# Performance work log

Measured on AMD Instinct MI355X. Metric: run time of the kernel, lower is better.

## Reference

```python
import jax, jax.numpy as jnp
import numpy as np

WIN = (7, 7)
NUM_HEADS = 6
DIM = 192
NW = 64          # windows per image
BATCH = 64       # images
B_ = BATCH * NW  # 4096 window-batches
N = WIN[0] * WIN[1]  # 49


def _relative_position_index():
    ch, cw = np.arange(WIN[0]), np.arange(WIN[1])
    coords = np.stack(np.meshgrid(ch, cw, indexing='ij'))          # [2, Wh, Ww]
    cf = coords.reshape(2, -1)                                      # [2, N]
    rel = cf[:, :, None] - cf[:, None, :]                           # [2, N, N]
    rel = rel.transpose(1, 2, 0).astype(np.int64)                   # [N, N, 2]
    rel[:, :, 0] += WIN[0] - 1
    rel[:, :, 1] += WIN[1] - 1
    rel[:, :, 0] *= 2 * WIN[1] - 1
    return rel.sum(-1).astype(np.int32)                             # [N, N]


def setup_inputs() -> dict:
    key = jax.random.key(0)
    ks = jax.random.split(key, 8)
    x = jax.random.normal(ks[0], (B_, N, DIM), dtype=jnp.float32)
    # additive shift-window mask: 0 where allowed, -100 where disallowed
    u = jax.random.uniform(ks[1], (NW, N, N))
    attn_mask = jnp.where(u < 0.15, -100.0, 0.0).astype(jnp.float32)
    rpb_table = jax.random.normal(ks[2], ((2 * WIN[0] - 1) * (2 * WIN[1] - 1), NUM_HEADS), dtype=jnp.float32) * 0.02
    rel_index = jnp.asarray(_relative_position_index())
    std = 1.0 / np.sqrt(DIM)
    qkv_w = jax.random.normal(ks[3], (3 * DIM, DIM), dtype=jnp.float32) * std
    qkv_b = jax.random.normal(ks[4], (3 * DIM,), dtype=jnp.float32) * 0.02
    proj_w = jax.random.normal(ks[5], (DIM, DIM), dtype=jnp.float32) * std
    proj_b = jax.random.normal(ks[6], (DIM,), dtype=jnp.float32) * 0.02
    return {"x": x, "attn_mask": attn_mask, "rpb_table": rpb_table,
            "rel_index": rel_index, "qkv_w": qkv_w, "qkv_b": qkv_b,
            "proj_w": proj_w, "proj_b": proj_b}


def reference(x, attn_mask, rpb_table, rel_index, qkv_w, qkv_b, proj_w, proj_b):
    Bw, n, C = x.shape
    H = NUM_HEADS
    hd = C // H
    scale = hd ** -0.5
    # qkv projection: [Bw, N, 3, H, hd] -> (3, Bw, H, N, hd)
    qkv = (x @ qkv_w.T + qkv_b).reshape(Bw, n, 3, H, hd).transpose(2, 0, 3, 1, 4)
    q, k, v = qkv[0], qkv[1], qkv[2]
    # gathered relative position bias: [H, N, N]
    rel_bias = rpb_table[rel_index.reshape(-1)].reshape(n, n, H).transpose(2, 0, 1)
    # scores [Bw, H, N, N]
    attn = jnp.einsum('bhnd,bhmd->bhnm', q * scale, k) + rel_bias[None]
    nW = attn_mask.shape[0]
    attn = attn.reshape(Bw // nW, nW, H, n, n) + attn_mask[None, :, None]
    attn = jax.nn.softmax(attn.reshape(Bw, H, n, n), axis=-1)
    out = jnp.einsum('bhnm,bhmd->bhnd', attn, v)  # [Bw, H, N, hd]
    out = out.transpose(0, 2, 1, 3).reshape(Bw, n, C)
    return out @ proj_w.T + proj_b
```

## Files before the change

### kernel.cpp

```cpp
#include <hip/hip_runtime.h>
#include <stdint.h>
#include <cmath>

typedef unsigned short ushort_t;
typedef __attribute__((ext_vector_type(8))) short bf16x8;
typedef __attribute__((ext_vector_type(4))) float f32x4;
typedef __attribute__((ext_vector_type(4))) unsigned int u32x4;

#define NTOK 49
#define DIMC 192
#define NH 6
#define HD 32
#define SCALE 0.17677669529663687f
#define LOG2E 1.4426950408889634f
#define LN2   0.6931471805599453f
#define XS 200
#define VTS 72
#define PS 72
#define MS 66
#define RS 68

#define OFF_X    0
#define OFF_Q    25600
#define OFF_K    51200
#define OFF_VT   76800
#define OFF_P    104448
#define OFF_MASK 122880
#define OFF_RPB  139776
#define OFF_REL  145184
#define OFF_BQ   153888
#define OFF_BP   156192
#define SMEM_BYTES 156960

#define QKVW_N (576 * 192)
#define PROJW_N (192 * 192)
#define QKV_GRP (4 * 9 * 6 * 64)
#define PROJ_GRP (4 * 3 * 6 * 64)
#define WBF_BYTES ((QKVW_N + PROJW_N) * 2)
#define BIAS_FLOATS (64 * 6 * 4 * 4 * 4 * 16 * 4)
#define WS_NEED1 ((size_t)WBF_BYTES)
#define WS_NEED2 ((size_t)WBF_BYTES + (size_t)BIAS_FLOATS * 4)

__device__ __forceinline__ ushort_t f2bf(float f) {
    uint32_t x = __builtin_bit_cast(uint32_t, f);
    x += 0x7fffu + ((x >> 16) & 1u);
    return (ushort_t)(x >> 16);
}
__device__ __forceinline__ uint32_t cvtpk(float lo, float hi) {
    uint32_t r;
    asm("v_cvt_pk_bf16_f32 %0, %1, %2" : "=v"(r) : "v"(lo), "v"(hi));
    return r;
}

__device__ __forceinline__ bf16x8 cvt8(const float* p) {
    f32x4 a = *(const f32x4*)p;
    f32x4 b = *(const f32x4*)(p + 4);
    bf16x8 r;
    r[0] = (short)f2bf(a[0]); r[1] = (short)f2bf(a[1]);
    r[2] = (short)f2bf(a[2]); r[3] = (short)f2bf(a[3]);
    r[4] = (short)f2bf(b[0]); r[5] = (short)f2bf(b[1]);
    r[6] = (short)f2bf(b[2]); r[7] = (short)f2bf(b[3]);
    return r;
}

__global__ __launch_bounds__(256) void swz_weights_kernel(
    const float* __restrict__ qkvw, const float* __restrict__ projw,
    ushort_t* __restrict__ dst)
{
    int i = blockIdx.x * 256 + threadIdx.x;
    if (i >= QKV_GRP + PROJ_GRP) return;
    const float* src;
    float s = 1.0f;
    if (i < QKV_GRP) {
        int lane = i & 63, t = i >> 6;
        int kk = t % 6, nt = (t / 6) % 9, cq = t / 54;
        int col = cq * 144 + nt * 16 + (lane & 15);
        int k0 = kk * 32 + (lane >> 4) * 8;
        src = qkvw + col * DIMC + k0;
        if (col < 192) s = SCALE * LOG2E;
    } else {
        int j = i - QKV_GRP;
        int lane = j & 63, t = j >> 6;
        int kk = t % 6, nt = (t / 6) % 3, cq = t / 18;
        int col = cq * 48 + nt * 16 + (lane & 15);
        int k0 = kk * 32 + (lane >> 4) * 8;
        src = projw + col * DIMC + k0;
    }
    f32x4 a = *(const f32x4*)src;
    f32x4 b = *(const f32x4*)(src + 4);
    u32x4 o;
    o[0] = (uint32_t)f2bf(a[0] * s) | ((uint32_t)f2bf(a[1] * s) << 16);
    o[1] = (uint32_t)f2bf(a[2] * s) | ((uint32_t)f2bf(a[3] * s) << 16);
    o[2] = (uint32_t)f2bf(b[0] * s) | ((uint32_t)f2bf(b[1] * s) << 16);
    o[3] = (uint32_t)f2bf(b[2] * s) | ((uint32_t)f2bf(b[3] * s) << 16);
    *(u32x4*)(dst + (size_t)i * 8) = o;
}

__global__ __launch_bounds__(256) void bias_kernel(
    const float* __restrict__ mask_g, const float* __restrict__ rpb_g,
    const int* __restrict__ rel_g, float* __restrict__ dst)
{
    int i = blockIdx.x * 256 + threadIdx.x;
    if (i >= BIAS_FLOATS / 4) return;
    int c = i & 15, g = (i >> 4) & 3, t = (i >> 6) & 3, wsid = (i >> 8) & 3;
    int hw = i >> 10;
    int h = hw % 6, wi = hw / 6;
    int m0 = 16 * wsid + 4 * g, n = 16 * t + c;
    f32x4 v;
    #pragma unroll
    for (int r = 0; r < 4; ++r) {
        int m = m0 + r;
        float val;
        if (n >= NTOK)      val = -30000.0f;
        else if (m >= NTOK) val = 0.0f;
        else val = mask_g[(size_t)wi * (NTOK * NTOK) + m * NTOK + n]
                 + rpb_g[(size_t)rel_g[m * NTOK + n] * NH + h];
        v[r] = val * LOG2E;
    }
    *(f32x4*)(dst + (size_t)i * 4) = v;
}

template <int MODE>
__global__ __launch_bounds__(512, 2) void win_attn_kernel(
    const float* __restrict__ x_g,
    const float* __restrict__ mask_g,
    const float* __restrict__ rpb_g,
    const int* __restrict__ rel_g,
    const float* __restrict__ qkvw_g,
    const float* __restrict__ qkvb_g,
    const float* __restrict__ projw_g,
    const float* __restrict__ projb_g,
    const ushort_t* __restrict__ wbf_g,
    const float* __restrict__ bias_g,
    float* __restrict__ out_g)
{
    extern __shared__ char smem[];
    ushort_t* x_lds  = (ushort_t*)(smem + OFF_X);
    ushort_t* q_lds  = (ushort_t*)(smem + OFF_Q);
    ushort_t* k_lds  = (ushort_t*)(smem + OFF_K);
    ushort_t* vT     = (ushort_t*)(smem + OFF_VT);
    ushort_t* P_lds  = (ushort_t*)(smem + OFF_P);
    float*    mask_p = (float*)(smem + OFF_MASK);
    float*    rpb_l  = (float*)(smem + OFF_RPB);
    ushort_t* rel_p  = (ushort_t*)(smem + OFF_REL);
    float*    bq     = (float*)(smem + OFF_BQ);
    float*    bp     = (float*)(smem + OFF_BP);

    const int tid  = threadIdx.x;
    const int b    = blockIdx.x;
    const int wi   = b & 63;
    const int w    = tid >> 6;
    const int lane = tid & 63;
    const int g    = lane >> 4;
    const int c    = lane & 15;

    bf16x8 ring[4][6];
    {
        if constexpr (MODE >= 1) {
            const int cq = w & 3;
            const ushort_t* wq = wbf_g + (size_t)cq * (9 * 6 * 64 * 8);
            #pragma unroll
            for (int p = 0; p < 3; ++p)
                #pragma unroll
                for (int kk = 0; kk < 6; ++kk)
                    ring[p][kk] = *(const bf16x8*)(wq + (size_t)((p * 6 + kk) * 64 + lane) * 8);
            __builtin_amdgcn_sched_barrier(0);
        }
    }

    {
        const float* xg = x_g + (size_t)b * (NTOK * DIMC);
        for (int i = tid; i < 64 * 24; i += 512) {
            int row = i / 24, col = (i % 24) * 8;
            u32x4 v = {0u, 0u, 0u, 0u};
            if (row < NTOK) {
                const float* src = xg + row * DIMC + col;
                f32x4 a = *(const f32x4*)src;
                f32x4 d = *(const f32x4*)(src + 4);
                v[0] = cvtpk(a[0], a[1]); v[1] = cvtpk(a[2], a[3]);
                v[2] = cvtpk(d[0], d[1]); v[3] = cvtpk(d[2], d[3]);
            }
            *(u32x4*)&x_lds[row * XS + col] = v;
        }
        if constexpr (MODE < 2) {
            const float* mw = mask_g + (size_t)wi * (NTOK * NTOK);
            for (int i = tid; i < 64 * 64; i += 512) {
                int m = i >> 6, n = i & 63;
                float f;
                if (n >= NTOK)      f = -30000.0f;
                else if (m >= NTOK) f = 0.0f;
                else                f = mw[m * NTOK + n];
                mask_p[m * MS + n] = f;
                rel_p[m * RS + n] = (m < NTOK && n < NTOK) ? (ushort_t)rel_g[m * NTOK + n]
                                                           : (ushort_t)0;
            }
            for (int i = tid; i < 169 * 6; i += 512)
                rpb_l[(i / 6) * 8 + (i % 6)] = rpb_g[i];
        }
        for (int i = tid; i < 576; i += 512) {
            float v = qkvb_g[i];
            if constexpr (MODE >= 1) { if (i < 192) v *= SCALE * LOG2E; }
            bq[i] = v;
        }
        if (tid < 192) bp[tid] = projb_g[tid];
    }
    __syncthreads();

    {
        const int mh = w >> 2, cq = w & 3;
        const ushort_t* wq = wbf_g + (size_t)cq * (9 * 6 * 64 * 8);

        bf16x8 ax[2][6];
        #pragma unroll
        for (int mt = 0; mt < 2; ++mt)
            #pragma unroll
            for (int kk = 0; kk < 6; ++kk)
                ax[mt][kk] = *(const bf16x8*)&x_lds[(32 * mh + 16 * mt + c) * XS + kk * 32 + g * 8];

        #pragma unroll
        for (int nt = 0; nt < 9; ++nt) {
            const int cg = 144 * cq + nt * 16 + c;
            bf16x8 bw[6];
            if constexpr (MODE >= 1) {
                if (nt + 3 < 9) {
                    #pragma unroll
                    for (int kk = 0; kk < 6; ++kk)
                        ring[(nt + 3) & 3][kk] =
                            *(const bf16x8*)(wq + (size_t)(((nt + 3) * 6 + kk) * 64 + lane) * 8);
                }
                __builtin_amdgcn_sched_barrier(0);
                #pragma unroll
                for (int kk = 0; kk < 6; ++kk) bw[kk] = ring[nt & 3][kk];
            } else {
                #pragma unroll
                for (int kk = 0; kk < 6; ++kk)
                    bw[kk] = cvt8(qkvw_g + (size_t)cg * DIMC + kk * 32 + g * 8);
            }
            const float bias = bq[cg];
            f32x4 acc[2];
            acc[0] = (f32x4){bias, bias, bias, bias};
            acc[1] = acc[0];
            #pragma unroll
            for (int kk = 0; kk < 6; ++kk)
                #pragma unroll
                for (int mt = 0; mt < 2; ++mt)
                    acc[mt] = __builtin_amdgcn_mfma_f32_16x16x32_bf16(ax[mt][kk], bw[kk], acc[mt], 0, 0, 0);

            const int seg = 144 * cq + nt * 16;
            if (seg < 192) {
                #pragma unroll
                for (int mt = 0; mt < 2; ++mt) {
                    uint32_t p01 = cvtpk(acc[mt][0], acc[mt][1]);
                    uint32_t p23 = cvtpk(acc[mt][2], acc[mt][3]);
                    const int r0 = 32 * mh + 16 * mt + g * 4;
                    q_lds[(r0 + 0) * XS + cg] = (ushort_t)p01;
                    q_lds[(r0 + 1) * XS + cg] = (ushort_t)(p01 >> 16);
                    q_lds[(r0 + 2) * XS + cg] = (ushort_t)p23;
                    q_lds[(r0 + 3) * XS + cg] = (ushort_t)(p23 >> 16);
                }
            } else if (seg < 384) {
                const int ck = cg - 192;
                #pragma unroll
                for (int mt = 0; mt < 2; ++mt) {
                    uint32_t p01 = cvtpk(acc[mt][0], acc[mt][1]);
                    uint32_t p23 = cvtpk(acc[mt][2], acc[mt][3]);
                    const int r0 = 32 * mh + 16 * mt + g * 4;
                    k_lds[(r0 + 0) * XS + ck] = (ushort_t)p01;
                    k_lds[(r0 + 1) * XS + ck] = (ushort_t)(p01 >> 16);
                    k_lds[(r0 + 2) * XS + ck] = (ushort_t)p23;
                    k_lds[(r0 + 3) * XS + ck] = (ushort_t)(p23 >> 16);
                }
            } else {
                const int cv = cg - 384;
                #pragma unroll
                for (int mt = 0; mt < 2; ++mt) {
                    uint32_t* dst = (uint32_t*)&vT[cv * VTS + 32 * mh + 16 * mt + g * 4];
                    dst[0] = cvtpk(acc[mt][0], acc[mt][1]);
                    dst[1] = cvtpk(acc[mt][2], acc[mt][3]);
                }
            }
        }
    }
    __syncthreads();

    bf16x8 pw[3][6];
    {
        const int wsid = w & 3, hh = w >> 2;
        ushort_t* Pw = P_lds + w * (16 * PS);
        const int mq0 = 16 * wsid + g * 4;

        if constexpr (MODE == 2) {
            const int h0 = hh * 3;
            f32x4 S0[4], S1[4], S2[4];
            const short oneb = (short)0x3F80;
            bf16x8 ones8 = {oneb, oneb, oneb, oneb, oneb, oneb, oneb, oneb};

            auto QKT = [&](int h, f32x4* S) {
                bf16x8 aq = *(const bf16x8*)&q_lds[(16 * wsid + c) * XS + h * HD + g * 8];
                const float* bC = bias_g + ((size_t)((wi * 6 + h) * 4 + wsid) * 4) * 256 + lane * 4;
                __builtin_amdgcn_s_setprio(1);
                #pragma unroll
                for (int t = 0; t < 4; ++t) {
                    f32x4 Ct = *(const f32x4*)(bC + t * 256);
                    bf16x8 bk = *(const bf16x8*)&k_lds[(16 * t + c) * XS + h * HD + g * 8];
                    S[t] = __builtin_amdgcn_mfma_f32_16x16x32_bf16(aq, bk, Ct, 0, 0, 0);
                }
                __builtin_amdgcn_s_setprio(0);
            };
            auto SM = [&](f32x4* S) {
                #pragma unroll
                for (int r = 0; r < 4; ++r) {
                    float e0 = exp2f(S[0][r]), e1 = exp2f(S[1][r]);
                    float e2 = exp2f(S[2][r]), e3 = exp2f(S[3][r]);
                    uint32_t p01 = cvtpk(e0, e1);
                    uint32_t p23 = cvtpk(e2, e3);
                    ushort_t* pr = Pw + (g * 4 + r) * PS + c;
                    pr[0]  = (ushort_t)p01;
                    pr[16] = (ushort_t)(p01 >> 16);
                    pr[32] = (ushort_t)p23;
                    pr[48] = (ushort_t)(p23 >> 16);
                }
            };
            auto PV = [&](int h) {
                f32x4 z = {0.f, 0.f, 0.f, 0.f};
                f32x4 O[2] = {z, z};
                f32x4 Osum = z;
                __builtin_amdgcn_s_setprio(1);
                #pragma unroll
                for (int ks = 0; ks < 2; ++ks) {
                    bf16x8 ap = *(const bf16x8*)&Pw[c * PS + ks * 32 + g * 8];
                    #pragma unroll
                    for (int nt = 0; nt < 2; ++nt) {
                        bf16x8 bv = *(const bf16x8*)&vT[(h * HD + nt * 16 + c) * VTS + ks * 32 + g * 8];
                        O[nt] = __builtin_amdgcn_mfma_f32_16x16x32_bf16(ap, bv, O[nt], 0, 0, 0);
                    }
                    Osum = __builtin_amdgcn_mfma_f32_16x16x32_bf16(ap, ones8, Osum, 0, 0, 0);
                }
                __builtin_amdgcn_s_setprio(0);
                #pragma unroll
                for (int r = 0; r < 4; ++r) {
                    float rinv = 1.0f / Osum[r];
                    uint32_t po = cvtpk(O[0][r] * rinv, O[1][r] * rinv);
                    ushort_t* ar = x_lds + (16 * wsid + g * 4 + r) * XS + h * HD + c;
                    ar[0]  = (ushort_t)po;
                    ar[16] = (ushort_t)(po >> 16);
                }
            };

            QKT(h0 + 0, S0);
            QKT(h0 + 1, S1);
            SM(S0);
            QKT(h0 + 2, S2);
            PV(h0 + 0);
            SM(S1);
            PV(h0 + 1);
            {
                const int cq4 = w & 3;
                const ushort_t* wp = wbf_g + QKVW_N + (size_t)cq4 * (3 * 6 * 64 * 8);
                #pragma unroll
                for (int nt = 0; nt < 3; ++nt)
                    #pragma unroll
                    for (int kk = 0; kk < 6; ++kk)
                        pw[nt][kk] = *(const bf16x8*)(wp + (size_t)((nt * 6 + kk) * 64 + lane) * 8);
                __builtin_amdgcn_sched_barrier(0);
            }
            SM(S2);
            PV(h0 + 2);
        } else {
            auto head = [&](int h) {
                bf16x8 aq = *(const bf16x8*)&q_lds[(16 * wsid + c) * XS + h * HD + g * 8];
                f32x4 S[4];
                #pragma unroll
                for (int t = 0; t < 4; ++t) {
                    bf16x8 bk = *(const bf16x8*)&k_lds[(16 * t + c) * XS + h * HD + g * 8];
                    f32x4 z = {0.f, 0.f, 0.f, 0.f};
                    S[t] = __builtin_amdgcn_mfma_f32_16x16x32_bf16(aq, bk, z, 0, 0, 0);
                }
                float rinv[4];
                #pragma unroll
                for (int r = 0; r < 4; ++r) {
                    const int mq = mq0 + r;
                    const float*    mrow = mask_p + mq * MS;
                    const ushort_t* rrow = rel_p + mq * RS;
                    float sv[4];
                    #pragma unroll
                    for (int t = 0; t < 4; ++t) {
                        const int n = 16 * t + c;
                        float sc = (MODE == 0) ? SCALE : LN2;
                        sv[t] = S[t][r] * sc + rpb_l[(int)rrow[n] * 8 + h] + mrow[n];
                    }
                    float vmax = fmaxf(fmaxf(sv[0], sv[1]), fmaxf(sv[2], sv[3]));
                    #pragma unroll
                    for (int xm = 1; xm < 16; xm <<= 1)
                        vmax = fmaxf(vmax, __shfl_xor(vmax, xm));
                    float sum = 0.f;
                    float ev[4];
                    #pragma unroll
                    for (int t = 0; t < 4; ++t) {
                        ev[t] = __expf(fmaxf(sv[t] - vmax, -80.0f));
                        sum += ev[t];
                    }
                    #pragma unroll
                    for (int xm = 1; xm < 16; xm <<= 1)
                        sum += __shfl_xor(sum, xm);
                    rinv[r] = 1.0f / sum;
                    uint32_t p01 = cvtpk(ev[0], ev[1]);
                    uint32_t p23 = cvtpk(ev[2], ev[3]);
                    ushort_t* pr = Pw + (g * 4 + r) * PS + c;
                    pr[0]  = (ushort_t)p01;
                    pr[16] = (ushort_t)(p01 >> 16);
                    pr[32] = (ushort_t)p23;
                    pr[48] = (ushort_t)(p23 >> 16);
                }
                f32x4 z = {0.f, 0.f, 0.f, 0.f};
                f32x4 O[2] = {z, z};
                #pragma unroll
                for (int ks = 0; ks < 2; ++ks) {
                    bf16x8 ap = *(const bf16x8*)&Pw[c * PS + ks * 32 + g * 8];
                    #pragma unroll
                    for (int nt = 0; nt < 2; ++nt) {
                        bf16x8 bv = *(const bf16x8*)&vT[(h * HD + nt * 16 + c) * VTS + ks * 32 + g * 8];
                        O[nt] = __builtin_amdgcn_mfma_f32_16x16x32_bf16(ap, bv, O[nt], 0, 0, 0);
                    }
                }
                #pragma unroll
                for (int r = 0; r < 4; ++r) {
                    uint32_t po = cvtpk(O[0][r] * rinv[r], O[1][r] * rinv[r]);
                    ushort_t* ar = x_lds + (16 * wsid + g * 4 + r) * XS + h * HD + c;
                    ar[0]  = (ushort_t)po;
                    ar[16] = (ushort_t)(po >> 16);
                }
            };
            head(hh * 3 + 0);
            head(hh * 3 + 1);
            if constexpr (MODE >= 1) {
                const int cq4 = w & 3;
                const ushort_t* wp = wbf_g + QKVW_N + (size_t)cq4 * (3 * 6 * 64 * 8);
                #pragma unroll
                for (int nt = 0; nt < 3; ++nt)
                    #pragma unroll
                    for (int kk = 0; kk < 6; ++kk)
                        pw[nt][kk] = *(const bf16x8*)(wp + (size_t)((nt * 6 + kk) * 64 + lane) * 8);
                __builtin_amdgcn_sched_barrier(0);
            }
            head(hh * 3 + 2);
        }
    }
    __syncthreads();

    {
        const int mh = w >> 2, cq4 = w & 3;
        bf16x8 aa[2][6];
        #pragma unroll
        for (int mt = 0; mt < 2; ++mt)
            #pragma unroll
            for (int kk = 0; kk < 6; ++kk)
                aa[mt][kk] = *(const bf16x8*)&x_lds[(32 * mh + 16 * mt + c) * XS + kk * 32 + g * 8];

        float* og = out_g + (size_t)b * (NTOK * DIMC);
        #pragma unroll
        for (int nt = 0; nt < 3; ++nt) {
            const int cg = 48 * cq4 + nt * 16 + c;
            bf16x8 bw[6];
            #pragma unroll
            for (int kk = 0; kk < 6; ++kk) {
                if constexpr (MODE >= 1)
                    bw[kk] = pw[nt][kk];
                else
                    bw[kk] = cvt8(projw_g + (size_t)cg * DIMC + kk * 32 + g * 8);
            }
            const float bias = bp[cg];
            f32x4 acc[2];
            acc[0] = (f32x4){bias, bias, bias, bias};
            acc[1] = acc[0];
            #pragma unroll
            for (int kk = 0; kk < 6; ++kk)
                #pragma unroll
                for (int mt = 0; mt < 2; ++mt)
                    acc[mt] = __builtin_amdgcn_mfma_f32_16x16x32_bf16(aa[mt][kk], bw[kk], acc[mt], 0, 0, 0);
            #pragma unroll
            for (int mt = 0; mt < 2; ++mt)
                #pragma unroll
                for (int r = 0; r < 4; ++r) {
                    const int row = 32 * mh + 16 * mt + g * 4 + r;
                    if (row < NTOK) og[row * DIMC + cg] = acc[mt][r];
                }
        }
    }
}

extern "C" void kernel_launch(void* const* d_in, const int* in_sizes, int n_in,
                              void* d_out, int out_size, void* d_ws, size_t ws_size,
                              hipStream_t stream) {
    (void)in_sizes; (void)n_in; (void)out_size;
    const float* x_g     = (const float*)d_in[0];
    const float* mask_g  = (const float*)d_in[1];
    const float* rpb_g   = (const float*)d_in[2];
    const int*   rel_g   = (const int*)d_in[3];
    const float* qkvw_g  = (const float*)d_in[4];
    const float* qkvb_g  = (const float*)d_in[5];
    const float* projw_g = (const float*)d_in[6];
    const float* projb_g = (const float*)d_in[7];
    float*       out_g   = (float*)d_out;

    const bool has_w = (d_ws != nullptr) && (ws_size >= WS_NEED1);
    const bool has_b = (d_ws != nullptr) && (ws_size >= WS_NEED2);
    ushort_t* wbf = (ushort_t*)d_ws;
    float* bias4 = (float*)((char*)d_ws + WBF_BYTES);

    if (has_w) {
        int ngrp = QKV_GRP + PROJ_GRP;
        hipLaunchKernelGGL(swz_weights_kernel, dim3((ngrp + 255) / 256), dim3(256), 0, stream,
                           qkvw_g, projw_g, wbf);
    }
    if (has_b) {
        int nthr = BIAS_FLOATS / 4;
        hipLaunchKernelGGL(bias_kernel, dim3((nthr + 255) / 256), dim3(256), 0, stream,
                           mask_g, rpb_g, rel_g, bias4);
        hipFuncSetAttribute((const void*)win_attn_kernel<2>,
                            hipFuncAttributeMaxDynamicSharedMemorySize, SMEM_BYTES);
        hipLaunchKernelGGL(win_attn_kernel<2>, dim3(4096), dim3(512), SMEM_BYTES, stream,
                           x_g, mask_g, rpb_g, rel_g, qkvw_g, qkvb_g, projw_g, projb_g,
                           wbf, bias4, out_g);
    } else if (has_w) {
        hipFuncSetAttribute((const void*)win_attn_kernel<1>,
                            hipFuncAttributeMaxDynamicSharedMemorySize, SMEM_BYTES);
        hipLaunchKernelGGL(win_attn_kernel<1>, dim3(4096), dim3(512), SMEM_BYTES, stream,
                           x_g, mask_g, rpb_g, rel_g, qkvw_g, qkvb_g, projw_g, projb_g,
                           wbf, (const float*)nullptr, out_g);
    } else {
        hipFuncSetAttribute((const void*)win_attn_kernel<0>,
                            hipFuncAttributeMaxDynamicSharedMemorySize, SMEM_BYTES);
        hipLaunchKernelGGL(win_attn_kernel<0>, dim3(4096), dim3(512), SMEM_BYTES, stream,
                           x_g, mask_g, rpb_g, rel_g, qkvw_g, qkvb_g, projw_g, projb_g,
                           (const ushort_t*)nullptr, (const float*)nullptr, out_g);
    }
}
```

Before: 205.7 us.

## Add dedicated 12-wave window-attention kernel with smaller LDS footprint

Replaces the MODE-2 template path with a new kernel using 768 threads (12 waves) per window. Each wave handles six 16-column tiles of the QKV projection, two heads of attention, and one 16-column slice of the output projection. The precomputed bias is used, so the mask, rel-index and rpb tables are no longer staged in LDS. This cuts shared memory from about 157KB to 135KB and spreads the per-window work over more waves, reducing the serial chain per wave. The trade-off is a launch bound of one 768-thread block per CU, which may lower occupancy relative to the previous two 512-thread blocks.

```diff
diff --git a/kernel.cpp b/kernel.cpp
--- a/kernel.cpp
+++ b/kernel.cpp
@@ -13,7 +13,6 @@
 #define HD 32
 #define SCALE 0.17677669529663687f
 #define LOG2E 1.4426950408889634f
-#define LN2   0.6931471805599453f
 #define XS 200
 #define VTS 72
 #define PS 72
@@ -25,12 +24,21 @@
 #define OFF_K    51200
 #define OFF_VT   76800
 #define OFF_P    104448
-#define OFF_MASK 122880
-#define OFF_RPB  139776
-#define OFF_REL  145184
-#define OFF_BQ   153888
-#define OFF_BP   156192
-#define SMEM_BYTES 156960
+#define OFF_BQ   132096
+#define OFF_BP   134400
+#define SMEM12   135168
+
+#define FOFF_X    0
+#define FOFF_Q    25600
+#define FOFF_K    51200
+#define FOFF_VT   76800
+#define FOFF_P    104448
+#define FOFF_MASK 122880
+#define FOFF_RPB  139776
+#define FOFF_REL  145184
+#define FOFF_BQ   153888
+#define FOFF_BP   156192
+#define FSMEM     156960
 
 #define QKVW_N (576 * 192)
 #define PROJW_N (192 * 192)
@@ -51,7 +59,6 @@
     asm("v_cvt_pk_bf16_f32 %0, %1, %2" : "=v"(r) : "v"(lo), "v"(hi));
     return r;
 }
-
 __device__ __forceinline__ bf16x8 cvt8(const float* p) {
     f32x4 a = *(const f32x4*)p;
     f32x4 b = *(const f32x4*)(p + 4);
@@ -120,6 +127,241 @@
     *(f32x4*)(dst + (size_t)i * 4) = v;
 }
 
+__global__ __launch_bounds__(768, 1) void win_attn12_kernel(
+    const float* __restrict__ x_g,
+    const float* __restrict__ qkvb_g,
+    const float* __restrict__ projb_g,
+    const ushort_t* __restrict__ wbf_g,
+    const float* __restrict__ bias_g,
+    float* __restrict__ out_g)
+{
+    extern __shared__ char smem[];
+    ushort_t* x_lds  = (ushort_t*)(smem + OFF_X);
+    ushort_t* q_lds  = (ushort_t*)(smem + OFF_Q);
+    ushort_t* k_lds  = (ushort_t*)(smem + OFF_K);
+    ushort_t* vT     = (ushort_t*)(smem + OFF_VT);
+    ushort_t* P_lds  = (ushort_t*)(smem + OFF_P);
+    float*    bq     = (float*)(smem + OFF_BQ);
+    float*    bp     = (float*)(smem + OFF_BP);
+
+    const int tid  = threadIdx.x;
+    const int b    = blockIdx.x;
+    const int wi   = b & 63;
+    const int w    = tid >> 6;
+    const int lane = tid & 63;
+    const int g    = lane >> 4;
+    const int c    = lane & 15;
+
+    const int mh = w / 6, cgrp = w % 6;
+    const int ct0 = 6 * cgrp;
+
+    bf16x8 ring[4][6];
+    #pragma unroll
+    for (int p = 0; p < 3; ++p)
+        #pragma unroll
+        for (int kk = 0; kk < 6; ++kk)
+            ring[p][kk] = *(const bf16x8*)(wbf_g + (size_t)(((ct0 + p) * 6 + kk) * 64 + lane) * 8);
+    __builtin_amdgcn_sched_barrier(0);
+
+    {
+        const float* xg = x_g + (size_t)b * (NTOK * DIMC);
+        for (int i = tid; i < 64 * 24; i += 768) {
+            int row = i / 24, col = (i % 24) * 8;
+            u32x4 v = {0u, 0u, 0u, 0u};
+            if (row < NTOK) {
+                const float* src = xg + row * DIMC + col;
+                f32x4 a = *(const f32x4*)src;
+                f32x4 d = *(const f32x4*)(src + 4);
+                v[0] = cvtpk(a[0], a[1]); v[1] = cvtpk(a[2], a[3]);
+                v[2] = cvtpk(d[0], d[1]); v[3] = cvtpk(d[2], d[3]);
+            }
+            *(u32x4*)&x_lds[row * XS + col] = v;
+        }
+        if (tid < 576) {
+            float v = qkvb_g[tid];
+            if (tid < 192) v *= SCALE * LOG2E;
+            bq[tid] = v;
+        }
+        if (tid < 192) bp[tid] = projb_g[tid];
+    }
+    __syncthreads();
+
+    {
+        bf16x8 ax[2][6];
+        #pragma unroll
+        for (int mt = 0; mt < 2; ++mt)
+            #pragma unroll
+            for (int kk = 0; kk < 6; ++kk)
+                ax[mt][kk] = *(const bf16x8*)&x_lds[(32 * mh + 16 * mt + c) * XS + kk * 32 + g * 8];
+
+        #pragma unroll
+        for (int i = 0; i < 6; ++i) {
+            const int ct = ct0 + i;
+            const int cg = ct * 16 + c;
+            if (i + 3 < 6) {
+                #pragma unroll
+                for (int kk = 0; kk < 6; ++kk)
+                    ring[(i + 3) & 3][kk] =
+                        *(const bf16x8*)(wbf_g + (size_t)(((ct0 + i + 3) * 6 + kk) * 64 + lane) * 8);
+            }
+            __builtin_amdgcn_sched_barrier(0);
+            bf16x8 bw[6];
+            #pragma unroll
+            for (int kk = 0; kk < 6; ++kk) bw[kk] = ring[i & 3][kk];
+
+            const float bias = bq[cg];
+            f32x4 acc[2];
+            acc[0] = (f32x4){bias, bias, bias, bias};
+            acc[1] = acc[0];
+            #pragma unroll
+            for (int kk = 0; kk < 6; ++kk)
+                #pragma unroll
+                for (int mt = 0; mt < 2; ++mt)
+                    acc[mt] = __builtin_amdgcn_mfma_f32_16x16x32_bf16(ax[mt][kk], bw[kk], acc[mt], 0, 0, 0);
+
+            if (cgrp < 2) {
+                #pragma unroll
+                for (int mt = 0; mt < 2; ++mt) {
+                    uint32_t p01 = cvtpk(acc[mt][0], acc[mt][1]);
+                    uint32_t p23 = cvtpk(acc[mt][2], acc[mt][3]);
+                    const int r0 = 32 * mh + 16 * mt + g * 4;
+                    q_lds[(r0 + 0) * XS + cg] = (ushort_t)p01;
+                    q_lds[(r0 + 1) * XS + cg] = (ushort_t)(p01 >> 16);
+                    q_lds[(r0 + 2) * XS + cg] = (ushort_t)p23;
+                    q_lds[(r0 + 3) * XS + cg] = (ushort_t)(p23 >> 16);
+                }
+            } else if (cgrp < 4) {
+                const int ck = cg - 192;
+                #pragma unroll
+                for (int mt = 0; mt < 2; ++mt) {
+                    uint32_t p01 = cvtpk(acc[mt][0], acc[mt][1]);
+                    uint32_t p23 = cvtpk(acc[mt][2], acc[mt][3]);
+                    const int r0 = 32 * mh + 16 * mt + g * 4;
+                    k_lds[(r0 + 0) * XS + ck] = (ushort_t)p01;
+                    k_lds[(r0 + 1) * XS + ck] = (ushort_t)(p01 >> 16);
+                    k_lds[(r0 + 2) * XS + ck] = (ushort_t)p23;
+                    k_lds[(r0 + 3) * XS + ck] = (ushort_t)(p23 >> 16);
+                }
+            } else {
+                const int cv = cg - 384;
+                #pragma unroll
+                for (int mt = 0; mt < 2; ++mt) {
+                    uint32_t* dst = (uint32_t*)&vT[cv * VTS + 32 * mh + 16 * mt + g * 4];
+                    dst[0] = cvtpk(acc[mt][0], acc[mt][1]);
+                    dst[1] = cvtpk(acc[mt][2], acc[mt][3]);
+                }
+            }
+        }
+    }
+    __syncthreads();
+
+    bf16x8 pw[6];
+    {
+        const int wsid = w & 3, hp = w >> 2;
+        ushort_t* Pw = P_lds + w * (16 * PS);
+        f32x4 S0[4], S1[4];
+        const short oneb = (short)0x3F80;
+        bf16x8 ones8 = {oneb, oneb, oneb, oneb, oneb, oneb, oneb, oneb};
+
+        auto QKT = [&](int h, f32x4* S) {
+            bf16x8 aq = *(const bf16x8*)&q_lds[(16 * wsid + c) * XS + h * HD + g * 8];
+            const float* bC = bias_g + ((size_t)((wi * 6 + h) * 4 + wsid) * 4) * 256 + lane * 4;
+            __builtin_amdgcn_s_setprio(1);
+            #pragma unroll
+            for (int t = 0; t < 4; ++t) {
+                f32x4 Ct = *(const f32x4*)(bC + t * 256);
+                bf16x8 bk = *(const bf16x8*)&k_lds[(16 * t + c) * XS + h * HD + g * 8];
+                S[t] = __builtin_amdgcn_mfma_f32_16x16x32_bf16(aq, bk, Ct, 0, 0, 0);
+            }
+            __builtin_amdgcn_s_setprio(0);
+        };
+        auto SM = [&](f32x4* S) {
+            #pragma unroll
+            for (int r = 0; r < 4; ++r) {
+                float e0 = exp2f(S[0][r]), e1 = exp2f(S[1][r]);
+                float e2 = exp2f(S[2][r]), e3 = exp2f(S[3][r]);
+                uint32_t p01 = cvtpk(e0, e1);
+                uint32_t p23 = cvtpk(e2, e3);
+                ushort_t* pr = Pw + (g * 4 + r) * PS + c;
+                pr[0]  = (ushort_t)p01;
+                pr[16] = (ushort_t)(p01 >> 16);
+                pr[32] = (ushort_t)p23;
+                pr[48] = (ushort_t)(p23 >> 16);
+            }
+        };
+        auto PV = [&](int h) {
+            f32x4 z = {0.f, 0.f, 0.f, 0.f};
+            f32x4 O[2] = {z, z};
+            f32x4 Osum = z;
+            __builtin_amdgcn_s_setprio(1);
+            #pragma unroll
+            for (int ks = 0; ks < 2; ++ks) {
+                bf16x8 ap = *(const bf16x8*)&Pw[c * PS + ks * 32 + g * 8];
+                #pragma unroll
+                for (int nt = 0; nt < 2; ++nt) {
+                    bf16x8 bv = *(const bf16x8*)&vT[(h * HD + nt * 16 + c) * VTS + ks * 32 + g * 8];
+                    O[nt] = __builtin_amdgcn_mfma_f32_16x16x32_bf16(ap, bv, O[nt], 0, 0, 0);
+                }
+                Osum = __builtin_amdgcn_mfma_f32_16x16x32_bf16(ap, ones8, Osum, 0, 0, 0);
+            }
+            __builtin_amdgcn_s_setprio(0);
+            #pragma unroll
+            for (int r = 0; r < 4; ++r) {
+                float rinv = 1.0f / Osum[r];
+                uint32_t po = cvtpk(O[0][r] * rinv, O[1][r] * rinv);
+                ushort_t* ar = x_lds + (16 * wsid + g * 4 + r) * XS + h * HD + c;
+                ar[0]  = (ushort_t)po;
+                ar[16] = (ushort_t)(po >> 16);
+            }
+        };
+
+        QKT(2 * hp + 0, S0);
+        QKT(2 * hp + 1, S1);
+        SM(S0);
+        PV(2 * hp + 0);
+        {
+            const ushort_t* wp = wbf_g + QKVW_N;
+            #pragma unroll
+            for (int kk = 0; kk < 6; ++kk)
+                pw[kk] = *(const bf16x8*)(wp + (size_t)((w * 6 + kk) * 64 + lane) * 8);
+            __builtin_amdgcn_sched_barrier(0);
+        }
+        SM(S1);
+        PV(2 * hp + 1);
+    }
+    __syncthreads();
+
+    {
+        const int cg = w * 16 + c;
+        const float bias = bp[cg];
+        float* og = out_g + (size_t)b * (NTOK * DIMC);
+        #pragma unroll
+        for (int mp = 0; mp < 2; ++mp) {
+            bf16x8 aa[2][6];
+            #pragma unroll
+            for (int mt = 0; mt < 2; ++mt)
+                #pragma unroll
+                for (int kk = 0; kk < 6; ++kk)
+                    aa[mt][kk] = *(const bf16x8*)&x_lds[(32 * mp + 16 * mt + c) * XS + kk * 32 + g * 8];
+            f32x4 acc[2];
+            acc[0] = (f32x4){bias, bias, bias, bias};
+            acc[1] = acc[0];
+            #pragma unroll
+            for (int kk = 0; kk < 6; ++kk)
+                #pragma unroll
+                for (int mt = 0; mt < 2; ++mt)
+                    acc[mt] = __builtin_amdgcn_mfma_f32_16x16x32_bf16(aa[mt][kk], pw[kk], acc[mt], 0, 0, 0);
+            #pragma unroll
+            for (int mt = 0; mt < 2; ++mt)
+                #pragma unroll
+                for (int r = 0; r < 4; ++r) {
+                    const int row = 32 * mp + 16 * mt + g * 4 + r;
+                    if (row < NTOK) og[row * DIMC + cg] = acc[mt][r];
+                }
+        }
+    }
+}
+
 template <int MODE>
 __global__ __launch_bounds__(512, 2) void win_attn_kernel(
     const float* __restrict__ x_g,
@@ -131,20 +373,19 @@
     const float* __restrict__ projw_g,
     const float* __restrict__ projb_g,
     const ushort_t* __restrict__ wbf_g,
-    const float* __restrict__ bias_g,
     float* __restrict__ out_g)
 {
     extern __shared__ char smem[];
-    ushort_t* x_lds  = (ushort_t*)(smem + OFF_X);
-    ushort_t* q_lds  = (ushort_t*)(smem + OFF_Q);
-    ushort_t* k_lds  = (ushort_t*)(smem + OFF_K);
-    ushort_t* vT     = (ushort_t*)(smem + OFF_VT);
-    ushort_t* P_lds  = (ushort_t*)(smem + OFF_P);
-    float*    mask_p = (float*)(smem + OFF_MASK);
-    float*    rpb_l  = (float*)(smem + OFF_RPB);
-    ushort_t* rel_p  = (ushort_t*)(smem + OFF_REL);
-    float*    bq     = (float*)(smem + OFF_BQ);
-    float*    bp     = (float*)(smem + OFF_BP);
+    ushort_t* x_lds  = (ushort_t*)(smem + FOFF_X);
+    ushort_t* q_lds  = (ushort_t*)(smem + FOFF_Q);
+    ushort_t* k_lds  = (ushort_t*)(smem + FOFF_K);
+    ushort_t* vT     = (ushort_t*)(smem + FOFF_VT);
+    ushort_t* P_lds  = (ushort_t*)(smem + FOFF_P);
+    float*    mask_p = (float*)(smem + FOFF_MASK);
+    float*    rpb_l  = (float*)(smem + FOFF_RPB);
+    ushort_t* rel_p  = (ushort_t*)(smem + FOFF_REL);
+    float*    bq     = (float*)(smem + FOFF_BQ);
+    float*    bp     = (float*)(smem + FOFF_BP);
 
     const int tid  = threadIdx.x;
     const int b    = blockIdx.x;
@@ -155,17 +396,15 @@
     const int c    = lane & 15;
 
     bf16x8 ring[4][6];
-    {
-        if constexpr (MODE >= 1) {
-            const int cq = w & 3;
-            const ushort_t* wq = wbf_g + (size_t)cq * (9 * 6 * 64 * 8);
-            #pragma unroll
-            for (int p = 0; p < 3; ++p)
-                #pragma unroll
-                for (int kk = 0; kk < 6; ++kk)
-                    ring[p][kk] = *(const bf16x8*)(wq + (size_t)((p * 6 + kk) * 64 + lane) * 8);
-            __builtin_amdgcn_sched_barrier(0);
-        }
+    if constexpr (MODE >= 1) {
+        const int cq = w & 3;
+        const ushort_t* wq = wbf_g + (size_t)cq * (9 * 6 * 64 * 8);
+        #pragma unroll
+        for (int p = 0; p < 3; ++p)
+            #pragma unroll
+            for (int kk = 0; kk < 6; ++kk)
+                ring[p][kk] = *(const bf16x8*)(wq + (size_t)((p * 6 + kk) * 64 + lane) * 8);
+        __builtin_amdgcn_sched_barrier(0);
     }
 
     {
@@ -182,21 +421,19 @@
             }
             *(u32x4*)&x_lds[row * XS + col] = v;
         }
-        if constexpr (MODE < 2) {
-            const float* mw = mask_g + (size_t)wi * (NTOK * NTOK);
-            for (int i = tid; i < 64 * 64; i += 512) {
-                int m = i >> 6, n = i & 63;
-                float f;
-                if (n >= NTOK)      f = -30000.0f;
-                else if (m >= NTOK) f = 0.0f;
-                else                f = mw[m * NTOK + n];
-                mask_p[m * MS + n] = f;
-                rel_p[m * RS + n] = (m < NTOK && n < NTOK) ? (ushort_t)rel_g[m * NTOK + n]
-                                                           : (ushort_t)0;
-            }
-            for (int i = tid; i < 169 * 6; i += 512)
-                rpb_l[(i / 6) * 8 + (i % 6)] = rpb_g[i];
-        }
+        const float* mw = mask_g + (size_t)wi * (NTOK * NTOK);
+        for (int i = tid; i < 64 * 64; i += 512) {
+            int m = i >> 6, n = i & 63;
+            float f;
+            if (n >= NTOK)      f = -30000.0f;
+            else if (m >= NTOK) f = 0.0f;
+            else                f = mw[m * NTOK + n];
+            mask_p[m * MS + n] = f;
+            rel_p[m * RS + n] = (m < NTOK && n < NTOK) ? (ushort_t)rel_g[m * NTOK + n]
+                                                       : (ushort_t)0;
+        }
+        for (int i = tid; i < 169 * 6; i += 512)
+            rpb_l[(i / 6) * 8 + (i % 6)] = rpb_g[i];
         for (int i = tid; i < 576; i += 512) {
             float v = qkvb_g[i];
             if constexpr (MODE >= 1) { if (i < 192) v *= SCALE * LOG2E; }
@@ -209,7 +446,6 @@
     {
         const int mh = w >> 2, cq = w & 3;
         const ushort_t* wq = wbf_g + (size_t)cq * (9 * 6 * 64 * 8);
-
         bf16x8 ax[2][6];
         #pragma unroll
         for (int mt = 0; mt < 2; ++mt)
@@ -288,163 +524,83 @@
         const int wsid = w & 3, hh = w >> 2;
         ushort_t* Pw = P_lds + w * (16 * PS);
         const int mq0 = 16 * wsid + g * 4;
-
-        if constexpr (MODE == 2) {
-            const int h0 = hh * 3;
-            f32x4 S0[4], S1[4], S2[4];
-            const short oneb = (short)0x3F80;
-            bf16x8 ones8 = {oneb, oneb, oneb, oneb, oneb, oneb, oneb, oneb};
-
-            auto QKT = [&](int h, f32x4* S) {
-                bf16x8 aq = *(const bf16x8*)&q_lds[(16 * wsid + c) * XS + h * HD + g * 8];
-                const float* bC = bias_g + ((size_t)((wi * 6 + h) * 4 + wsid) * 4) * 256 + lane * 4;
-                __builtin_amdgcn_s_setprio(1);
+        auto head = [&](int h) {
+            bf16x8 aq = *(const bf16x8*)&q_lds[(16 * wsid + c) * XS + h * HD + g * 8];
+            f32x4 S[4];
+            #pragma unroll
+            for (int t = 0; t < 4; ++t) {
+                bf16x8 bk = *(const bf16x8*)&k_lds[(16 * t + c) * XS + h * HD + g * 8];
+                f32x4 z = {0.f, 0.f, 0.f, 0.f};
+                S[t] = __builtin_amdgcn_mfma_f32_16x16x32_bf16(aq, bk, z, 0, 0, 0);
+            }
+            float rinv[4];
+            #pragma unroll
+            for (int r = 0; r < 4; ++r) {
+                const int mq = mq0 + r;
+                const float*    mrow = mask_p + mq * MS;
+                const ushort_t* rrow = rel_p + mq * RS;
+                float sv[4];
                 #pragma unroll
                 for (int t = 0; t < 4; ++t) {
-                    f32x4 Ct = *(const f32x4*)(bC + t * 256);
-                    bf16x8 bk = *(const bf16x8*)&k_lds[(16 * t + c) * XS + h * HD + g * 8];
-                    S[t] = __builtin_amdgcn_mfma_f32_16x16x32_bf16(aq, bk, Ct, 0, 0, 0);
-                }
-                __builtin_amdgcn_s_setprio(0);
-            };
-            auto SM = [&](f32x4* S) {
-                #pragma unroll
-                for (int r = 0; r < 4; ++r) {
-                    float e0 = exp2f(S[0][r]), e1 = exp2f(S[1][r]);
-                    float e2 = exp2f(S[2][r]), e3 = exp2f(S[3][r]);
-                    uint32_t p01 = cvtpk(e0, e1);
-                    uint32_t p23 = cvtpk(e2, e3);
-                    ushort_t* pr = Pw + (g * 4 + r) * PS + c;
-                    pr[0]  = (ushort_t)p01;
-                    pr[16] = (ushort_t)(p01 >> 16);
-                    pr[32] = (ushort_t)p23;
-                    pr[48] = (ushort_t)(p23 >> 16);
-                }
-            };
-            auto PV = [&](int h) {
-                f32x4 z = {0.f, 0.f, 0.f, 0.f};
-                f32x4 O[2] = {z, z};
-                f32x4 Osum = z;
-                __builtin_amdgcn_s_setprio(1);
-                #pragma unroll
-                for (int ks = 0; ks < 2; ++ks) {
-                    bf16x8 ap = *(const bf16x8*)&Pw[c * PS + ks * 32 + g * 8];
-                    #pragma unroll
-                    for (int nt = 0; nt < 2; ++nt) {
-                        bf16x8 bv = *(const bf16x8*)&vT[(h * HD + nt * 16 + c) * VTS + ks * 32 + g * 8];
-                        O[nt] = __builtin_amdgcn_mfma_f32_16x16x32_bf16(ap, bv, O[nt], 0, 0, 0);
-                    }
-                    Osum = __builtin_amdgcn_mfma_f32_16x16x32_bf16(ap, ones8, Osum, 0, 0, 0);
-                }
-                __builtin_amdgcn_s_setprio(0);
-                #pragma unroll
-                for (int r = 0; r < 4; ++r) {
-                    float rinv = 1.0f / Osum[r];
-                    uint32_t po = cvtpk(O[0][r] * rinv, O[1][r] * rinv);
-                    ushort_t* ar = x_lds + (16 * wsid + g * 4 + r) * XS + h * HD + c;
-                    ar[0]  = (ushort_t)po;
-                    ar[16] = (ushort_t)(po >> 16);
-                }
-            };
-
-            QKT(h0 + 0, S0);
-            QKT(h0 + 1, S1);
-            SM(S0);
-            QKT(h0 + 2, S2);
-            PV(h0 + 0);
-            SM(S1);
-            PV(h0 + 1);
-            {
-                const int cq4 = w & 3;
-                const ushort_t* wp = wbf_g + QKVW_N + (size_t)cq4 * (3 * 6 * 64 * 8);
-                #pragma unroll
-                for (int nt = 0; nt < 3; ++nt)
-                    #pragma unroll
-                    for (int kk = 0; kk < 6; ++kk)
-                        pw[nt][kk] = *(const bf16x8*)(wp + (size_t)((nt * 6 + kk) * 64 + lane) * 8);
-                __builtin_amdgcn_sched_barrier(0);
-            }
-            SM(S2);
-            PV(h0 + 2);
-        } else {
-            auto head = [&](int h) {
-                bf16x8 aq = *(const bf16x8*)&q_lds[(16 * wsid + c) * XS + h * HD + g * 8];
-                f32x4 S[4];
+                    const int n = 16 * t + c;
+                    float sc = (MODE == 0) ? SCALE : 0.6931471805599453f;
+                    sv[t] = S[t][r] * sc + rpb_l[(int)rrow[n] * 8 + h] + mrow[n];
+                }
+                float vmax = fmaxf(fmaxf(sv[0], sv[1]), fmaxf(sv[2], sv[3]));
+                #pragma unroll
+                for (int xm = 1; xm < 16; xm <<= 1)
+                    vmax = fmaxf(vmax, __shfl_xor(vmax, xm));
+                float sum = 0.f;
+                float ev[4];
                 #pragma unroll
                 for (int t = 0; t < 4; ++t) {
-                    bf16x8 bk = *(const bf16x8*)&k_lds[(16 * t + c) * XS + h * HD + g * 8];
-                    f32x4 z = {0.f, 0.f, 0.f, 0.f};
-                    S[t] = __builtin_amdgcn_mfma_f32_16x16x32_bf16(aq, bk, z, 0, 0, 0);
-                }
-                float rinv[4];
-                #pragma unroll
-                for (int r = 0; r < 4; ++r) {
-                    const int mq = mq0 + r;
-                    const float*    mrow = mask_p + mq * MS;
-                    const ushort_t* rrow = rel_p + mq * RS;
-                    float sv[4];
-                    #pragma unroll
-                    for (int t = 0; t < 4; ++t) {
-                        const int n = 16 * t + c;
-                        float sc = (MODE == 0) ? SCALE : LN2;
-                        sv[t] = S[t][r] * sc + rpb_l[(int)rrow[n] * 8 + h] + mrow[n];
-                    }
-                    float vmax = fmaxf(fmaxf(sv[0], sv[1]), fmaxf(sv[2], sv[3]));
-                    #pragma unroll
-                    for (int xm = 1; xm < 16; xm <<= 1)
-                        vmax = fmaxf(vmax, __shfl_xor(vmax, xm));
-                    float sum = 0.f;
-                    float ev[4];
-                    #pragma unroll
-                    for (int t = 0; t < 4; ++t) {
-                        ev[t] = __expf(fmaxf(sv[t] - vmax, -80.0f));
-                        sum += ev[t];
-                    }
-                    #pragma unroll
-                    for (int xm = 1; xm < 16; xm <<= 1)
-                        sum += __shfl_xor(sum, xm);
-                    rinv[r] = 1.0f / sum;
-                    uint32_t p01 = cvtpk(ev[0], ev[1]);
-                    uint32_t p23 = cvtpk(ev[2], ev[3]);
-                    ushort_t* pr = Pw + (g * 4 + r) * PS + c;
-                    pr[0]  = (ushort_t)p01;
-                    pr[16] = (ushort_t)(p01 >> 16);
-                    pr[32] = (ushort_t)p23;
-                    pr[48] = (ushort_t)(p23 >> 16);
-                }
-                f32x4 z = {0.f, 0.f, 0.f, 0.f};
-                f32x4 O[2] = {z, z};
-                #pragma unroll
-                for (int ks = 0; ks < 2; ++ks) {
-                    bf16x8 ap = *(const bf16x8*)&Pw[c * PS + ks * 32 + g * 8];
-                    #pragma unroll
-                    for (int nt = 0; nt < 2; ++nt) {
-                        bf16x8 bv = *(const bf16x8*)&vT[(h * HD + nt * 16 + c) * VTS + ks * 32 + g * 8];
-                        O[nt] = __builtin_amdgcn_mfma_f32_16x16x32_bf16(ap, bv, O[nt], 0, 0, 0);
-                    }
-                }
-                #pragma unroll
-                for (int r = 0; r < 4; ++r) {
-                    uint32_t po = cvtpk(O[0][r] * rinv[r], O[1][r] * rinv[r]);
-                    ushort_t* ar = x_lds + (16 * wsid + g * 4 + r) * XS + h * HD + c;
-                    ar[0]  = (ushort_t)po;
-                    ar[16] = (ushort_t)(po >> 16);
-                }
-            };
-            head(hh * 3 + 0);
-            head(hh * 3 + 1);
-            if constexpr (MODE >= 1) {
-                const int cq4 = w & 3;
-                const ushort_t* wp = wbf_g + QKVW_N + (size_t)cq4 * (3 * 6 * 64 * 8);
-                #pragma unroll
-                for (int nt = 0; nt < 3; ++nt)
-                    #pragma unroll
-                    for (int kk = 0; kk < 6; ++kk)
-                        pw[nt][kk] = *(const bf16x8*)(wp + (size_t)((nt * 6 + kk) * 64 + lane) * 8);
-                __builtin_amdgcn_sched_barrier(0);
-            }
-            head(hh * 3 + 2);
-        }
+                    ev[t] = __expf(fmaxf(sv[t] - vmax, -80.0f));
+                    sum += ev[t];
+                }
+                #pragma unroll
+                for (int xm = 1; xm < 16; xm <<= 1)
+                    sum += __shfl_xor(sum, xm);
+                rinv[r] = 1.0f / sum;
+                uint32_t p01 = cvtpk(ev[0], ev[1]);
+                uint32_t p23 = cvtpk(ev[2], ev[3]);
+                ushort_t* pr = Pw + (g * 4 + r) * PS + c;
+                pr[0]  = (ushort_t)p01;
+                pr[16] = (ushort_t)(p01 >> 16);
+                pr[32] = (ushort_t)p23;
+                pr[48] = (ushort_t)(p23 >> 16);
+            }
+            f32x4 z = {0.f, 0.f, 0.f, 0.f};
+            f32x4 O[2] = {z, z};
+            #pragma unroll
+            for (int ks = 0; ks < 2; ++ks) {
+                bf16x8 ap = *(const bf16x8*)&Pw[c * PS + ks * 32 + g * 8];
+                #pragma unroll
+                for (int nt = 0; nt < 2; ++nt) {
+                    bf16x8 bv = *(const bf16x8*)&vT[(h * HD + nt * 16 + c) * VTS + ks * 32 + g * 8];
+                    O[nt] = __builtin_amdgcn_mfma_f32_16x16x32_bf16(ap, bv, O[nt], 0, 0, 0);
+                }
+            }
+            #pragma unroll
+            for (int r = 0; r < 4; ++r) {
+                uint32_t po = cvtpk(O[0][r] * rinv[r], O[1][r] * rinv[r]);
+                ushort_t* ar = x_lds + (16 * wsid + g * 4 + r) * XS + h * HD + c;
+                ar[0]  = (ushort_t)po;
+                ar[16] = (ushort_t)(po >> 16);
+            }
+        };
+        head(hh * 3 + 0);
+        head(hh * 3 + 1);
+        if constexpr (MODE >= 1) {
+            const int cq4 = w & 3;
+            const ushort_t* wp = wbf_g + QKVW_N + (size_t)cq4 * (3 * 6 * 64 * 8);
+            #pragma unroll
+            for (int nt = 0; nt < 3; ++nt)
+                #pragma unroll
+                for (int kk = 0; kk < 6; ++kk)
+                    pw[nt][kk] = *(const bf16x8*)(wp + (size_t)((nt * 6 + kk) * 64 + lane) * 8);
+            __builtin_amdgcn_sched_barrier(0);
+        }
+        head(hh * 3 + 2);
     }
     __syncthreads();
 
@@ -517,22 +673,21 @@
         int nthr = BIAS_FLOATS / 4;
         hipLaunchKernelGGL(bias_kernel, dim3((nthr + 255) / 256), dim3(256), 0, stream,
                            mask_g, rpb_g, rel_g, bias4);
-        hipFuncSetAttribute((const void*)win_attn_kernel<2>,
-                            hipFuncAttributeMaxDynamicSharedMemorySize, SMEM_BYTES);
-        hipLaunchKernelGGL(win_attn_kernel<2>, dim3(4096), dim3(512), SMEM_BYTES, stream,
-                           x_g, mask_g, rpb_g, rel_g, qkvw_g, qkvb_g, projw_g, projb_g,
-                           wbf, bias4, out_g);
+        hipFuncSetAttribute((const void*)win_attn12_kernel,
+                            hipFuncAttributeMaxDynamicSharedMemorySize, SMEM12);
+        hipLaunchKernelGGL(win_attn12_kernel, dim3(4096), dim3(768), SMEM12, stream,
+                           x_g, qkvb_g, projb_g, wbf, bias4, out_g);
     } else if (has_w) {
         hipFuncSetAttribute((const void*)win_attn_kernel<1>,
-                            hipFuncAttributeMaxDynamicSharedMemorySize, SMEM_BYTES);
-        hipLaunchKernelGGL(win_attn_kernel<1>, dim3(4096), dim3(512), SMEM_BYTES, stream,
+                            hipFuncAttributeMaxDynamicSharedMemorySize, FSMEM);
+        hipLaunchKernelGGL(win_attn_kernel<1>, dim3(4096), dim3(512), FSMEM, stream,
                            x_g, mask_g, rpb_g, rel_g, qkvw_g, qkvb_g, projw_g, projb_g,
-                           wbf, (const float*)nullptr, out_g);
+                           wbf, out_g);
     } else {
         hipFuncSetAttribute((const void*)win_attn_kernel<0>,
-                            hipFuncAttributeMaxDynamicSharedMemorySize, SMEM_BYTES);
-        hipLaunchKernelGGL(win_attn_kernel<0>, dim3(4096), dim3(512), SMEM_BYTES, stream,
+                            hipFuncAttributeMaxDynamicSharedMemorySize, FSMEM);
+        hipLaunchKernelGGL(win_attn_kernel<0>, dim3(4096), dim3(512), FSMEM, stream,
                            x_g, mask_g, rpb_g, rel_g, qkvw_g, qkvb_g, projw_g, projb_g,
-                           (const ushort_t*)nullptr, (const float*)nullptr, out_g);
-    }
-}
+                           (const ushort_t*)nullptr, out_g);
+    }
+}
```

New measurement: 202.4 us, median of 2. No clear change (-1.6%).
